# Performance work log

Hardware: AMD Instinct MI355X
Metric: run time of the kernel (lower is better)

Reference implementation:

```python
import jax, jax.numpy as jnp
import numpy as np

# Izhikevich params (regular spiking), Euler step with dt=1
A, B_P, C, D, V_TH, DT = 0.02, 0.2, -65.0, 8.0, 30.0, 1.0


def _izh_scan(currents):
    """Run an Izhikevich cell over time. currents: [T, B, F] -> spikes [T, B, F]."""
    shp = currents.shape[1:]
    v0 = jnp.full(shp, C, dtype=currents.dtype)
    u0 = jnp.full(shp, B_P * C, dtype=currents.dtype)

    def step(state, i_t):
        v, u = state
        v = v + DT * (0.04 * v * v + 5.0 * v + 140.0 - u + i_t)
        u = u + DT * A * (B_P * v - u)
        z = (v >= V_TH).astype(currents.dtype)  # spike (heaviside)
        v = jnp.where(z > 0, C, v)               # reset
        u = u + z * D
        return (v, u), z

    (vT, uT), spikes = jax.lax.scan(step, (v0, u0), currents)
    return spikes, (vT, uT)


def setup_inputs() -> dict:
    key = jax.random.key(0)
    k1, k2, k3, k4, k5 = jax.random.split(key, 5)
    T, B, F_IN, F_HID = 2048, 8192, 4, 2
    xs = jax.random.normal(k1, (T, B, F_IN), dtype=jnp.float32)
    # PyTorch Linear default init: U(-1/sqrt(fan_in), 1/sqrt(fan_in)); scaled normal is fine for a baseline
    W_in = jax.random.normal(k2, (F_HID, F_IN), dtype=jnp.float32) * 0.5
    b_in = jax.random.normal(k3, (F_HID,), dtype=jnp.float32) * 0.5
    W_out = jax.random.normal(k4, (1, F_HID), dtype=jnp.float32) * 0.5
    b_out = jax.random.normal(k5, (1,), dtype=jnp.float32) * 0.5
    return {"xs": xs, "W_in": W_in, "b_in": b_in, "W_out": W_out, "b_out": b_out}


def reference(xs, W_in, b_in, W_out, b_out):
    # input linear: [T,B,4] @ [4,2] -> [T,B,2]
    h = jnp.einsum('tbi,oi->tbo', xs, W_in) + b_in
    input_spikes, _ = _izh_scan(h)
    # output linear: [T,B,2] -> [T,B,1]
    y = jnp.einsum('tbi,oi->tbo', input_spikes, W_out) + b_out
    output_spikes, _ = _izh_scan(y)
    return output_spikes
```

## Files before the change

### kernel.cpp

```cpp
#include <hip/hip_runtime.h>

namespace {

constexpr int T   = 2048;
constexpr int B   = 8192;
constexpr int C   = 16;
constexpr int NCH = T / C;
constexpr int NB  = 4;

__device__ __forceinline__ void barrier_nodrain() {
    asm volatile("s_waitcnt lgkmcnt(0)\n\ts_barrier" ::: "memory");
}

struct IzhState {
    float vnp;
    float up;
    bool  spp;
};

__device__ __forceinline__ bool izh_step(IzhState& s, float I) {
#pragma clang fp contract(off)
    const float K0 = ((0.04f * (-65.0f)) * (-65.0f) + (5.0f * (-65.0f))) + 140.0f;
    float m2a = 0.04f * s.vnp;
    float m2  = m2a * s.vnp;
    float f5  = 5.0f * s.vnp;
    float s2A = (m2 + f5) + 140.0f;
    float s3A = s2A - s.up;
    float s4A = s3A + I;
    float vnA = s.vnp + s4A;
    float s3S = K0 - s.up;
    float s4S = s3S + I;
    float vnS = (-65.0f) + s4S;
    float vn  = s.spp ? vnS : vnA;
    bool  sp  = (vn >= 30.0f);
    float m4  = 0.2f * vn;
    float s5  = m4 - s.up;
    float tt  = 0.02f * s5;
    float un  = s.up + tt;
    float d8  = sp ? 8.0f : 0.0f;
    s.up  = un + d8;
    s.vnp = vn;
    s.spp = sp;
    return sp;
}

__global__ __launch_bounds__(320, 1) void izh5(
    const float* __restrict__ xs,
    const float* __restrict__ W_in, const float* __restrict__ b_in,
    const float* __restrict__ W_out, const float* __restrict__ b_out,
    float* __restrict__ out)
{
    __shared__ float hbuf[2][NB][C][64];
    __shared__ float sbuf[2][2][C][64];

    const int lane = threadIdx.x & 63;
    const int wid  = threadIdx.x >> 6;
    const int b    = blockIdx.x * 64 + lane;

    if (wid >= 3) {
#pragma clang fp contract(off)
        const int w = wid - 3;
        const float w00 = W_in[0], w01 = W_in[1], w02 = W_in[2], w03 = W_in[3];
        const float w10 = W_in[4], w11 = W_in[5], w12 = W_in[6], w13 = W_in[7];
        const float bi0 = b_in[0], bi1 = b_in[1];
        const float4* xp = reinterpret_cast<const float4*>(xs) + b;

        auto fill = [&](int m) {
#pragma clang fp contract(off)
            const int slot = m & (NB - 1);
            float4 xv[C];
#pragma unroll
            for (int j = 0; j < C; ++j) xv[j] = xp[(size_t)(m * C + j) * B];
#pragma unroll
            for (int j = 0; j < C; ++j) {
                const float4 x = xv[j];
                float h0 = (((x.x * w00) + (x.y * w01)) + (x.z * w02)) + (x.w * w03);
                h0 = h0 + bi0;
                float h1 = (((x.x * w10) + (x.y * w11)) + (x.z * w12)) + (x.w * w13);
                h1 = h1 + bi1;
                hbuf[0][slot][j][lane] = h0;
                hbuf[1][slot][j][lane] = h1;
            }
        };

        fill(w);
        barrier_nodrain();
        for (int r = 0; r <= NCH; ++r) {
            const int m = r + 2;
            if (m < NCH && (m & 1) == w) fill(m);
            barrier_nodrain();
        }
    } else if (wid < 2) {
#pragma clang fp contract(off)
        IzhState st{-65.0f, -13.0f, true};
        barrier_nodrain();
        for (int r = 0; r <= NCH; ++r) {
            if (r < NCH) {
                const int slot = r & (NB - 1);
                const int par  = r & 1;
                float Iv[C];
#pragma unroll
                for (int j = 0; j < C; ++j) Iv[j] = hbuf[wid][slot][j][lane];
#pragma unroll
                for (int j = 0; j < C; ++j) {
                    bool sp = izh_step(st, Iv[j]);
                    sbuf[wid][par][j][lane] = sp ? 1.0f : 0.0f;
                }
            }
            barrier_nodrain();
        }
    } else {
#pragma clang fp contract(off)
        const float wo0 = W_out[0], wo1 = W_out[1], bo = b_out[0];
        const float c00 = ((0.0f * wo0) + (0.0f * wo1)) + bo;
        const float c10 = ((1.0f * wo0) + (0.0f * wo1)) + bo;
        const float c01 = ((0.0f * wo0) + (1.0f * wo1)) + bo;
        const float c11 = ((1.0f * wo0) + (1.0f * wo1)) + bo;
        float* op = out + b;
        IzhState st{-65.0f, -13.0f, true};
        barrier_nodrain();
        for (int r = 0; r <= NCH; ++r) {
            if (r >= 1) {
                const int c   = r - 1;
                const int par = c & 1;
                float z0[C], z1[C];
#pragma unroll
                for (int j = 0; j < C; ++j) {
                    z0[j] = sbuf[0][par][j][lane];
                    z1[j] = sbuf[1][par][j][lane];
                }
#pragma unroll
                for (int j = 0; j < C; ++j) {
                    float yt = (z1[j] != 0.0f) ? c11 : c10;
                    float yf = (z1[j] != 0.0f) ? c01 : c00;
                    float y  = (z0[j] != 0.0f) ? yt : yf;
                    bool spo = izh_step(st, y);
                    op[(size_t)(c * C + j) * B] = spo ? 1.0f : 0.0f;
                }
            }
            barrier_nodrain();
        }
    }
}

}

extern "C" void kernel_launch(void* const* d_in, const int* in_sizes, int n_in,
                              void* d_out, int out_size, void* d_ws, size_t ws_size,
                              hipStream_t stream) {
    const float* xs    = (const float*)d_in[0];
    const float* W_in  = (const float*)d_in[1];
    const float* b_in  = (const float*)d_in[2];
    const float* W_out = (const float*)d_in[3];
    const float* b_out = (const float*)d_in[4];
    float* out = (float*)d_out;

    dim3 grid(B / 64), block(320);
    hipLaunchKernelGGL(izh5, grid, block, 0, stream,
                       xs, W_in, b_in, W_out, b_out, out);
}
```

Before: 445.3 us.

## Merge loader waves into hidden-neuron waves with register ring prefetch

The two dedicated loader waves and their shared-memory h buffer are removed. Each hidden-neuron wave now computes its own input projection directly and prefetches xs through a 16-deep register ring. The chunk size doubles to 32 timesteps, which halves the number of block barriers, and the block shrinks from 5 waves to 3. The risk is that global load latency now sits on the serial recurrence path of the hidden waves, and that more registers are used per wave. The ring index wraps modulo T, so the last iterations issue harmless redundant loads.

```diff
diff --git a/kernel.cpp b/kernel.cpp
--- a/kernel.cpp
+++ b/kernel.cpp
@@ -4,9 +4,9 @@
 
 constexpr int T   = 2048;
 constexpr int B   = 8192;
-constexpr int C   = 16;
+constexpr int C   = 32;
 constexpr int NCH = T / C;
-constexpr int NB  = 4;
+constexpr int RD  = 16;
 
 __device__ __forceinline__ void barrier_nodrain() {
     asm volatile("s_waitcnt lgkmcnt(0)\n\ts_barrier" ::: "memory");
@@ -44,68 +44,40 @@
     return sp;
 }
 
-__global__ __launch_bounds__(320, 1) void izh5(
+__global__ __launch_bounds__(192, 1) void izh3b(
     const float* __restrict__ xs,
     const float* __restrict__ W_in, const float* __restrict__ b_in,
     const float* __restrict__ W_out, const float* __restrict__ b_out,
     float* __restrict__ out)
 {
-    __shared__ float hbuf[2][NB][C][64];
-    __shared__ float sbuf[2][2][C][64];
-
+    __shared__ float zbuf[2][2][C][64];
     const int lane = threadIdx.x & 63;
     const int wid  = threadIdx.x >> 6;
     const int b    = blockIdx.x * 64 + lane;
 
-    if (wid >= 3) {
+    if (wid < 2) {
 #pragma clang fp contract(off)
-        const int w = wid - 3;
-        const float w00 = W_in[0], w01 = W_in[1], w02 = W_in[2], w03 = W_in[3];
-        const float w10 = W_in[4], w11 = W_in[5], w12 = W_in[6], w13 = W_in[7];
-        const float bi0 = b_in[0], bi1 = b_in[1];
+        const float wa = W_in[wid * 4 + 0], wb = W_in[wid * 4 + 1];
+        const float wc = W_in[wid * 4 + 2], wd = W_in[wid * 4 + 3];
+        const float bi = b_in[wid];
         const float4* xp = reinterpret_cast<const float4*>(xs) + b;
 
-        auto fill = [&](int m) {
-#pragma clang fp contract(off)
-            const int slot = m & (NB - 1);
-            float4 xv[C];
+        float4 ring[RD];
 #pragma unroll
-            for (int j = 0; j < C; ++j) xv[j] = xp[(size_t)(m * C + j) * B];
+        for (int i = 0; i < RD; ++i) ring[i] = xp[(size_t)i * B];
+
+        IzhState st{-65.0f, -13.0f, true};
+        for (int r = 0; r < NCH; ++r) {
+            const int p = r & 1;
 #pragma unroll
             for (int j = 0; j < C; ++j) {
-                const float4 x = xv[j];
-                float h0 = (((x.x * w00) + (x.y * w01)) + (x.z * w02)) + (x.w * w03);
-                h0 = h0 + bi0;
-                float h1 = (((x.x * w10) + (x.y * w11)) + (x.z * w12)) + (x.w * w13);
-                h1 = h1 + bi1;
-                hbuf[0][slot][j][lane] = h0;
-                hbuf[1][slot][j][lane] = h1;
-            }
-        };
-
-        fill(w);
-        barrier_nodrain();
-        for (int r = 0; r <= NCH; ++r) {
-            const int m = r + 2;
-            if (m < NCH && (m & 1) == w) fill(m);
-            barrier_nodrain();
-        }
-    } else if (wid < 2) {
-#pragma clang fp contract(off)
-        IzhState st{-65.0f, -13.0f, true};
-        barrier_nodrain();
-        for (int r = 0; r <= NCH; ++r) {
-            if (r < NCH) {
-                const int slot = r & (NB - 1);
-                const int par  = r & 1;
-                float Iv[C];
-#pragma unroll
-                for (int j = 0; j < C; ++j) Iv[j] = hbuf[wid][slot][j][lane];
-#pragma unroll
-                for (int j = 0; j < C; ++j) {
-                    bool sp = izh_step(st, Iv[j]);
-                    sbuf[wid][par][j][lane] = sp ? 1.0f : 0.0f;
-                }
+                const int t = r * C + j;
+                const float4 x = ring[j & (RD - 1)];
+                ring[j & (RD - 1)] = xp[(size_t)((t + RD) & (T - 1)) * B];
+                float h = (((x.x * wa) + (x.y * wb)) + (x.z * wc)) + (x.w * wd);
+                h = h + bi;
+                bool sp = izh_step(st, h);
+                zbuf[wid][p][j][lane] = sp ? 1.0f : 0.0f;
             }
             barrier_nodrain();
         }
@@ -118,28 +90,31 @@
         const float c11 = ((1.0f * wo0) + (1.0f * wo1)) + bo;
         float* op = out + b;
         IzhState st{-65.0f, -13.0f, true};
-        barrier_nodrain();
-        for (int r = 0; r <= NCH; ++r) {
-            if (r >= 1) {
-                const int c   = r - 1;
-                const int par = c & 1;
-                float z0[C], z1[C];
+
+        auto consume = [&](int kk) {
+#pragma clang fp contract(off)
+            const int p = kk & 1;
+            float z0[C], z1[C];
 #pragma unroll
-                for (int j = 0; j < C; ++j) {
-                    z0[j] = sbuf[0][par][j][lane];
-                    z1[j] = sbuf[1][par][j][lane];
-                }
+            for (int j = 0; j < C; ++j) {
+                z0[j] = zbuf[0][p][j][lane];
+                z1[j] = zbuf[1][p][j][lane];
+            }
 #pragma unroll
-                for (int j = 0; j < C; ++j) {
-                    float yt = (z1[j] != 0.0f) ? c11 : c10;
-                    float yf = (z1[j] != 0.0f) ? c01 : c00;
-                    float y  = (z0[j] != 0.0f) ? yt : yf;
-                    bool spo = izh_step(st, y);
-                    op[(size_t)(c * C + j) * B] = spo ? 1.0f : 0.0f;
-                }
+            for (int j = 0; j < C; ++j) {
+                float yt = (z1[j] != 0.0f) ? c11 : c10;
+                float yf = (z1[j] != 0.0f) ? c01 : c00;
+                float y  = (z0[j] != 0.0f) ? yt : yf;
+                bool spo = izh_step(st, y);
+                op[(size_t)(kk * C + j) * B] = spo ? 1.0f : 0.0f;
             }
+        };
+
+        for (int r = 0; r < NCH; ++r) {
+            if (r > 0) consume(r - 1);
             barrier_nodrain();
         }
+        consume(NCH - 1);
     }
 }
 
@@ -155,7 +130,7 @@
     const float* b_out = (const float*)d_in[4];
     float* out = (float*)d_out;
 
-    dim3 grid(B / 64), block(320);
-    hipLaunchKernelGGL(izh5, grid, block, 0, stream,
+    dim3 grid(B / 64), block(192);
+    hipLaunchKernelGGL(izh3b, grid, block, 0, stream,
                        xs, W_in, b_in, W_out, b_out, out);
 }
```

After: 431.5 us. 3.1% less time.
